# Performance work log

Measured on AMD Instinct MI355X. Metric: run time of the kernel, lower is better.

Reference implementation:

```python
import jax, jax.numpy as jnp
import numpy as np

# ---- Cl(3,0) algebra tables (basis: 1, e1, e2, e3, e12, e13, e23, e123) ----
def _build_algebra():
    dim = 8
    blades = sorted(range(dim), key=lambda b: (bin(b).count('1'), b))
    idx = {b: i for i, b in enumerate(blades)}
    C = np.zeros((dim, dim, dim), np.float32)
    for a in range(dim):
        for b in range(dim):
            s = 0; ash = a >> 1
            while ash:
                s += bin(ash & b).count('1'); ash >>= 1
            C[idx[a], idx[b], idx[a ^ b]] = -1.0 if (s & 1) else 1.0
    grades = np.array([bin(b).count('1') for b in blades])
    rev = np.array([(-1.0) ** (g * (g - 1) // 2) for g in grades], np.float32)
    gmask = np.zeros((4, dim), np.float32)
    gmask[grades, np.arange(dim)] = 1.0
    return C, rev, gmask, grades

_C_np, _REV_np, _GM_np, _GRADES = _build_algebra()
CAYLEY = jnp.asarray(_C_np)          # [8,8,8] sparse multiplication table
REV = jnp.asarray(_REV_np)           # reverse signs per blade
GMASK = jnp.asarray(_GM_np)          # [4,8] grade selector
BV_IDX = jnp.asarray(np.where(_GRADES == 2)[0])  # bivector slots [4,5,6]
G1_IDX = jnp.asarray(np.where(_GRADES == 1)[0])  # vector slots [1,2,3]

EPS = 1e-6
H_NUM, DEPTH, A_NUM, DISC, TEMP = 8, 3, 5, 0.99, 1.0

def gp(a, b):
    return jnp.einsum('...i,...j,ijk->...k', a, b, CAYLEY)

def reverse(x):
    return x * REV

def grade_energy(x):  # [...,8] -> [...,4] per-grade sum of squares
    return jnp.einsum('...d,gd->...g', x * x, GMASK)

def scatter_bv(c):  # [...,3] bivector coeffs -> full multivector [...,8]
    out = jnp.zeros(c.shape[:-1] + (8,), c.dtype)
    return out.at[..., BV_IDX].set(c)

def mv_exp_biv(b):  # exp of pure bivector in Cl(3,0): cos|B| + sinc|B| * B
    t = jnp.sqrt(jnp.sum(b * b, -1))
    small = t < 1e-6
    ts = jnp.where(small, 1.0, t)
    sinc = jnp.where(small, 1.0 - t * t / 6.0, jnp.sin(ts) / ts)
    return (sinc[..., None] * b).at[..., 0].add(jnp.cos(t))

def clayernorm(x, w):  # normalize by mean multivector norm across channels
    n = jnp.sqrt(jnp.sum(x * x, -1) + EPS)          # [...,C]
    denom = jnp.mean(n, -1, keepdims=True)[..., None] + EPS
    return x * w[:, None] / denom

def ggelu(x):  # gate multivector by GELU of its norm
    n = jnp.sqrt(jnp.sum(x * x, -1, keepdims=True) + EPS)
    return x * jax.nn.gelu(n) / (n + EPS)

def clinear(x, W, b):  # channel-mixing per blade: [O,C]x[...,C,8]
    return jnp.einsum('oc,...cd->...od', W, x) + b

def rotor_apply(x, bv):  # per-channel rotor sandwich, bv [C,3]
    R = mv_exp_biv(-0.5 * scatter_bv(bv))  # [C,8]
    return gp(gp(R, x), reverse(R))

def predict(x, nw, lw, lb, vw, vb, pw, pb):
    h = clayernorm(x, nw)
    h = clinear(h, lw, lb)
    h = ggelu(h)
    value = h[..., 0] @ vw + vb                      # grade-0 -> [N,1]
    g1 = h[..., G1_IDX].reshape(h.shape[0], -1)       # grade-1 flat
    policy = g1 @ pw + pb                             # [N,A]
    return policy, value

def dynamics(x, action, act_bv, nw, rbv, lw, lb, rw, rb):
    bv = act_bv[action]                               # [N,3]
    R = mv_exp_biv(-0.5 * scatter_bv(bv))[:, None, :]  # [N,1,8]
    ns = gp(gp(R, x), reverse(R))                     # rotor sandwich
    h = clayernorm(ns, nw)
    h = ggelu(h)
    h = rotor_apply(h, rbv)
    h = clinear(h, lw, lb)
    ns = ns + h                                       # residual GA block
    reward = ns[..., 0] @ rw + rb
    return reward, ns


def setup_inputs() -> dict:
    key = jax.random.key(0)
    ks = jax.random.split(key, 16)
    B, C, mid = 512, 256, 128
    f = jnp.float32
    return {
        'state': jax.random.normal(ks[0], (B, C, 8), f),
        'hyp_bv': jax.random.normal(ks[1], (H_NUM, 3), f) * 0.05,
        'sp_w1': jax.random.normal(ks[2], (4, 32), f) * 0.3,
        'sp_b1': jnp.zeros((32,), f),
        'sp_w2': jax.random.normal(ks[3], (32, 1), f) * 0.3,
        'sp_b2': jnp.zeros((1,), f),
        'p_norm_w': jnp.ones((C,), f),
        'p_lin_w': jax.random.normal(ks[4], (mid, C), f) / np.sqrt(C),
        'p_lin_b': jnp.zeros((mid, 8), f),
        'p_vw': jax.random.normal(ks[5], (mid, 1), f) * 0.1,
        'p_vb': jnp.zeros((1,), f),
        'p_pw': jax.random.normal(ks[6], (mid * 3, A_NUM), f) * 0.1,
        'p_pb': jnp.zeros((A_NUM,), f),
        'act_bv': jax.random.normal(ks[7], (A_NUM, 3), f) * 0.1,
        'd_norm_w': jnp.ones((C,), f),
        'd_rotor_bv': jax.random.normal(ks[8], (C, 3), f) * 0.05,
        'd_lin_w': jax.random.normal(ks[9], (C, C), f) / np.sqrt(C),
        'd_lin_b': jnp.zeros((C, 8), f),
        'd_rw': jax.random.normal(ks[10], (C, 1), f) * 0.1,
        'd_rb': jnp.zeros((1,), f),
    }


def reference(state, hyp_bv, sp_w1, sp_b1, sp_w2, sp_b2,
              p_norm_w, p_lin_w, p_lin_b, p_vw, p_vb, p_pw, p_pb,
              act_bv, d_norm_w, d_rotor_bv, d_lin_w, d_lin_b, d_rw, d_rb):
    B, C, D = state.shape
    H, A = H_NUM, A_NUM
    # hypothesis generation: H independent rotors applied to state
    R = mv_exp_biv(-0.5 * scatter_bv(hyp_bv))          # [H,8]
    hyp = gp(gp(R[None, :, None, :], state[:, None, :, :]),
             reverse(R)[None, :, None, :])             # [B,H,C,8]
    # exploration parameter from grade-norm features
    norms = jnp.sqrt(grade_energy(state) + 1e-12)       # [B,C,4]
    pooled = norms.mean(1)                              # [B,4]
    theta = jnp.maximum(pooled @ sp_w1 + sp_b1, 0.0) @ sp_w2 + sp_b2
    explore = jnp.abs(jnp.tanh(theta))                  # [B,1]
    N = B * H
    hf = hyp.reshape(N, C, D)
    exp_bh = jnp.broadcast_to(explore[:, None, :], (B, H, 1)).reshape(N, 1)
    noise = jax.random.normal(jax.random.key(42), (DEPTH, N, A), state.dtype) * 0.3
    hyp_values = jnp.zeros((B, H), state.dtype)
    first_actions = jnp.zeros((N,), jnp.int32)
    for d in range(DEPTH):  # fixed small depth loop; H vectorized
        policy, value = predict(hf, p_norm_w, p_lin_w, p_lin_b, p_vw, p_vb, p_pw, p_pb)
        bv_e = grade_energy(hf)[:, :, 2].mean(1, keepdims=True)  # bivector energy
        scores = policy + exp_bh * bv_e * noise[d]
        action = jnp.argmax(scores, -1)
        if d == 0:
            first_actions = action
        reward, hf = dynamics(hf, action, act_bv, d_norm_w, d_rotor_bv,
                              d_lin_w, d_lin_b, d_rw, d_rb)
        hyp_values = hyp_values + (DISC ** d) * reward.reshape(B, H)
    _, tv = predict(hf, p_norm_w, p_lin_w, p_lin_b, p_vw, p_vb, p_pw, p_pb)
    hyp_values = hyp_values + (DISC ** DEPTH) * tv.reshape(B, H)
    weights = jax.nn.softmax(hyp_values / TEMP, -1)     # [B,H]
    oh = jax.nn.one_hot(first_actions.reshape(B, H), A, dtype=state.dtype)
    ap = jnp.sum(weights[..., None] * oh, 1)            # [B,A]
    return ap / jnp.clip(jnp.sum(ap, -1, keepdims=True), 1e-8)
```

## Files before the change

### kernel.cpp

```cpp
#include <hip/hip_runtime.h>
#include <math.h>


#define NOISE_MODE 0
#define DEV static __device__ __forceinline__

constexpr int Bz = 512;
constexpr int Cz = 256;
constexpr int MIDz = 128;
constexpr int Hz = 8;
constexpr int Nz = 4096;
constexpr int Az = 5;
constexpr int NOISE_PER_D = Nz * Az;

constexpr size_t OFF_ROTH  = 0;
constexpr size_t OFF_ROTA  = OFF_ROTH + 64;
constexpr size_t OFF_ROTC  = OFF_ROTA + 40;
constexpr size_t OFF_EXPL  = OFF_ROTC + 2048;
constexpr size_t OFF_HV    = OFF_EXPL + 512;
constexpr size_t OFF_FIRST = OFF_HV + 4096;
constexpr size_t OFF_WTP   = OFF_FIRST + 4096;
constexpr size_t OFF_WTD   = OFF_WTP + (size_t)Cz * MIDz;
constexpr size_t OFF_A     = OFF_WTD + (size_t)Cz * Cz;

DEV void gp8(const float* a, const float* b, float* c) {
  c[0] = a[0]*b[0]+a[1]*b[1]+a[2]*b[2]+a[3]*b[3]-a[4]*b[4]-a[5]*b[5]-a[6]*b[6]-a[7]*b[7];
  c[1] = a[0]*b[1]+a[1]*b[0]-a[2]*b[4]-a[3]*b[5]+a[4]*b[2]+a[5]*b[3]-a[6]*b[7]-a[7]*b[6];
  c[2] = a[0]*b[2]+a[2]*b[0]+a[1]*b[4]-a[4]*b[1]-a[3]*b[6]+a[6]*b[3]+a[5]*b[7]+a[7]*b[5];
  c[3] = a[0]*b[3]+a[3]*b[0]+a[1]*b[5]-a[5]*b[1]+a[2]*b[6]-a[6]*b[2]-a[4]*b[7]-a[7]*b[4];
  c[4] = a[0]*b[4]+a[4]*b[0]+a[1]*b[2]-a[2]*b[1]-a[5]*b[6]+a[6]*b[5]+a[3]*b[7]+a[7]*b[3];
  c[5] = a[0]*b[5]+a[5]*b[0]+a[1]*b[3]-a[3]*b[1]+a[4]*b[6]-a[6]*b[4]-a[2]*b[7]-a[7]*b[2];
  c[6] = a[0]*b[6]+a[6]*b[0]+a[2]*b[3]-a[3]*b[2]-a[4]*b[5]+a[5]*b[4]+a[1]*b[7]+a[7]*b[1];
  c[7] = a[0]*b[7]+a[7]*b[0]+a[1]*b[6]+a[6]*b[1]+a[3]*b[4]+a[4]*b[3]-a[2]*b[5]-a[5]*b[2];
}

DEV void sandwich8(const float* R, const float* x, float* y) {
  float t[8];
  gp8(R, x, t);
  float Rr[8] = {R[0], R[1], R[2], R[3], -R[4], -R[5], -R[6], -R[7]};
  gp8(t, Rr, y);
}

DEV void rotor_from_bv(const float* bv, float* R) {
  float c4 = -0.5f * bv[0], c5 = -0.5f * bv[1], c6 = -0.5f * bv[2];
  float t = sqrtf(c4*c4 + c5*c5 + c6*c6);
  float sinc = (t < 1e-6f) ? (1.0f - t*t/6.0f) : (sinf(t)/t);
  R[0] = cosf(t); R[1] = 0.f; R[2] = 0.f; R[3] = 0.f;
  R[4] = sinc*c4; R[5] = sinc*c5; R[6] = sinc*c6; R[7] = 0.f;
}

DEV unsigned tf_rotl(unsigned v, int n) { return (v << n) | (v >> (32 - n)); }

DEV void threefry2x32(unsigned x0, unsigned x1, unsigned& o0, unsigned& o1) {
  const unsigned k0 = 0u, k1 = 42u;
  const unsigned k2 = k0 ^ k1 ^ 0x1BD11BDAu;
  x0 += k0; x1 += k1;
#define TF_R(r) { x0 += x1; x1 = tf_rotl(x1, r); x1 ^= x0; }
  TF_R(13) TF_R(15) TF_R(26) TF_R(6)
  x0 += k1; x1 += k2 + 1u;
  TF_R(17) TF_R(29) TF_R(16) TF_R(24)
  x0 += k2; x1 += k0 + 2u;
  TF_R(13) TF_R(15) TF_R(26) TF_R(6)
  x0 += k0; x1 += k1 + 3u;
  TF_R(17) TF_R(29) TF_R(16) TF_R(24)
  x0 += k1; x1 += k2 + 4u;
  TF_R(13) TF_R(15) TF_R(26) TF_R(6)
  x0 += k2; x1 += k0 + 5u;
#undef TF_R
  o0 = x0; o1 = x1;
}

DEV float erfinv32(float x) {
  float w = -log1pf(-x * x);
  float p;
  if (w < 5.0f) {
    w = w - 2.5f;
    p = 2.81022636e-08f;
    p = fmaf(p, w, 3.43273939e-07f);
    p = fmaf(p, w, -3.5233877e-06f);
    p = fmaf(p, w, -4.39150654e-06f);
    p = fmaf(p, w, 0.00021858087f);
    p = fmaf(p, w, -0.00125372503f);
    p = fmaf(p, w, -0.00417768164f);
    p = fmaf(p, w, 0.246640727f);
    p = fmaf(p, w, 1.50140941f);
  } else {
    w = sqrtf(w) - 3.0f;
    p = -0.000200214257f;
    p = fmaf(p, w, 0.000100950558f);
    p = fmaf(p, w, 0.00134934322f);
    p = fmaf(p, w, -0.00367342844f);
    p = fmaf(p, w, 0.00573950773f);
    p = fmaf(p, w, -0.0076224613f);
    p = fmaf(p, w, 0.00943887047f);
    p = fmaf(p, w, 1.00167406f);
    p = fmaf(p, w, 2.83297682f);
  }
  return p * x;
}

DEV float noise_val(int d, int r, int a) {
  unsigned idx = (unsigned)(d * NOISE_PER_D + r * Az + a);
  unsigned o0, o1, bits;
#if NOISE_MODE == 0
  threefry2x32(0u, idx, o0, o1);
  bits = o0 ^ o1;
#elif NOISE_MODE == 1
  const unsigned HALF = (unsigned)(3 * NOISE_PER_D) / 2u;
  unsigned j = (idx < HALF) ? idx : idx - HALF;
  threefry2x32(j, j + HALF, o0, o1);
  bits = (idx < HALF) ? o0 : o1;
#elif NOISE_MODE == 2
  threefry2x32(0u, idx, o0, o1);
  bits = o1;
#else
  threefry2x32(0u, idx, o0, o1);
  bits = o0;
#endif
  const float MINV = __uint_as_float(0xBF7FFFFFu);
  float f = __uint_as_float((bits >> 9) | 0x3F800000u) - 1.0f;
  float u = fmaxf(MINV, f * 2.0f + MINV);
  const float SQRT2 = __uint_as_float(0x3FB504F3u);
  return (SQRT2 * erfinv32(u)) * 0.3f;
}

DEV float gelu_tanh(float x) {
  float x3 = (x * x) * x;
  float t = tanhf(0.7978845608028654f * (x + 0.044715f * x3));
  return x * (0.5f * (1.0f + t));
}

DEV void pred_gemm(const float4* __restrict__ X, int l, float invd,
                   const float* __restrict__ WtP, const float* __restrict__ plb,
                   float hh[2][8]) {
  float pacc[2][8] = {{0,0,0,0,0,0,0,0},{0,0,0,0,0,0,0,0}};
  const float2* Wp2 = (const float2*)WtP;
#pragma unroll 4
  for (int c = 0; c < Cz; c++) {
    float4 xa = X[c], xb = X[Cz + c];
    float xv[8] = {xa.x, xa.y, xa.z, xa.w, xb.x, xb.y, xb.z, xb.w};
    float2 wv = Wp2[(size_t)c * 64 + l];
#pragma unroll
    for (int dd = 0; dd < 8; dd++) {
      pacc[0][dd] = fmaf(wv.x, xv[dd], pacc[0][dd]);
      pacc[1][dd] = fmaf(wv.y, xv[dd], pacc[1][dd]);
    }
  }
#pragma unroll
  for (int j = 0; j < 2; j++) {
    int o = 2 * l + j;
    float nsq = 0.f;
#pragma unroll
    for (int dd = 0; dd < 8; dd++) {
      hh[j][dd] = fmaf(pacc[j][dd], invd, plb[o * 8 + dd]);
      nsq += hh[j][dd] * hh[j][dd];
    }
    float nn = sqrtf(nsq + 1e-6f);
    float sc = gelu_tanh(nn) / (nn + 1e-6f);
#pragma unroll
    for (int dd = 0; dd < 8; dd++) hh[j][dd] *= sc;
  }
}


__global__ void k_prep(const float* __restrict__ hyp_bv, const float* __restrict__ act_bv,
                       const float* __restrict__ rot_bv, const float* __restrict__ plw,
                       const float* __restrict__ pnw, const float* __restrict__ dlw,
                       float* __restrict__ rotH, float* __restrict__ rotA,
                       float* __restrict__ rotC, float* __restrict__ hyp_val,
                       float* __restrict__ WtP, float* __restrict__ WtD) {
  int t = blockIdx.x * 256 + threadIdx.x;
  if (t < Cz * Cz)   { int c = t >> 8, o = t & 255; WtD[t] = dlw[o * Cz + c]; }
  if (t < Cz * MIDz) { int c = t >> 7, o = t & 127; WtP[t] = plw[o * Cz + c] * pnw[c]; }
  if (t < Nz) hyp_val[t] = 0.f;
  if (t < 8) rotor_from_bv(hyp_bv + t * 3, rotH + t * 8);
  else if (t < 13) rotor_from_bv(act_bv + (t - 8) * 3, rotA + (t - 8) * 8);
  else if (t >= 16 && t < 16 + Cz) rotor_from_bv(rot_bv + (t - 16) * 3, rotC + (t - 16) * 8);
}

__global__ void k_explore(const float* __restrict__ state, const float* __restrict__ w1,
                          const float* __restrict__ b1, const float* __restrict__ w2,
                          const float* __restrict__ b2, float* __restrict__ explore) {
  int b = blockIdx.x, c = threadIdx.x;
  const float4* xp = (const float4*)(state + ((size_t)b * Cz + c) * 8);
  float4 lo = xp[0], hi = xp[1];
  float g0 = lo.x * lo.x;
  float g1 = lo.y * lo.y + lo.z * lo.z + lo.w * lo.w;
  float g2 = hi.x * hi.x + hi.y * hi.y + hi.z * hi.z;
  float g3 = hi.w * hi.w;
  __shared__ float4 sm[256];
  sm[c] = make_float4(sqrtf(g0 + 1e-12f), sqrtf(g1 + 1e-12f),
                      sqrtf(g2 + 1e-12f), sqrtf(g3 + 1e-12f));
  __syncthreads();
  for (int s = 128; s > 0; s >>= 1) {
    if (c < s) {
      sm[c].x += sm[c + s].x; sm[c].y += sm[c + s].y;
      sm[c].z += sm[c + s].z; sm[c].w += sm[c + s].w;
    }
    __syncthreads();
  }
  if (c == 0) {
    float pooled[4] = {sm[0].x / 256.f, sm[0].y / 256.f, sm[0].z / 256.f, sm[0].w / 256.f};
    float theta = b2[0];
    for (int j = 0; j < 32; j++) {
      float hj = b1[j];
      for (int g = 0; g < 4; g++) hj = fmaf(pooled[g], w1[g * 32 + j], hj);
      hj = fmaxf(hj, 0.f);
      theta = fmaf(hj, w2[j], theta);
    }
    explore[b] = fabsf(tanhf(theta));
  }
}

__global__ __launch_bounds__(256, 4) void k_step(
    const float* __restrict__ src, float* __restrict__ dst, int apply_hyp,
    int dstep, int do_term,
    const float* __restrict__ rotH, const float* __restrict__ rotA,
    const float* __restrict__ rotC, const float* __restrict__ WtP,
    const float* __restrict__ plb, const float* __restrict__ pw,
    const float* __restrict__ pb, const float* __restrict__ vw,
    const float* __restrict__ vb, const float* __restrict__ dnw,
    const float* __restrict__ WtD, const float* __restrict__ dlb,
    const float* __restrict__ rw, const float* __restrict__ rb,
    const float* __restrict__ explore, float* __restrict__ hyp_val,
    int* __restrict__ first_act, float discf, float termdisc) {
  __shared__ float4 xs[4][2 * Cz];
  int w = threadIdx.x >> 6, l = threadIdx.x & 63;
  int r = blockIdx.x * 4 + w;
  int b = r >> 3, h = r & 7;
  float4* X = xs[w];
  const float* row = apply_hyp ? (src + (size_t)b * Cz * 8) : (src + (size_t)r * Cz * 8);
  float Rh[8];
  if (apply_hyp) {
#pragma unroll
    for (int i = 0; i < 8; i++) Rh[i] = rotH[h * 8 + i];
  }
  float nsum = 0.f, bsum = 0.f;
#pragma unroll
  for (int k = 0; k < 4; k++) {
    int c = 4 * l + k;
    const float4* xp = (const float4*)(row + (size_t)c * 8);
    float4 v0 = xp[0], v1 = xp[1];
    float x[8] = {v0.x, v0.y, v0.z, v0.w, v1.x, v1.y, v1.z, v1.w};
    if (apply_hyp) {
      float t[8];
      sandwich8(Rh, x, t);
#pragma unroll
      for (int i = 0; i < 8; i++) x[i] = t[i];
    }
    float ss = 0.f;
#pragma unroll
    for (int i = 0; i < 8; i++) ss += x[i] * x[i];
    nsum += sqrtf(ss + 1e-6f);
    bsum += x[4] * x[4] + x[5] * x[5] + x[6] * x[6];
    X[c]      = make_float4(x[0], x[1], x[2], x[3]);
    X[Cz + c] = make_float4(x[4], x[5], x[6], x[7]);
  }
#pragma unroll
  for (int m = 1; m < 64; m <<= 1) {
    nsum += __shfl_xor(nsum, m);
    bsum += __shfl_xor(bsum, m);
  }
  float invd = 1.0f / (nsum / 256.f + 1e-6f);
  float bv_e = bsum / 256.f;
  __syncthreads();

  float hh[2][8];
  pred_gemm(X, l, invd, WtP, plb, hh);
  float pol[Az] = {0, 0, 0, 0, 0};
#pragma unroll
  for (int j = 0; j < 2; j++) {
    int o = 2 * l + j;
#pragma unroll
    for (int k = 0; k < 3; k++) {
      float v = hh[j][1 + k];
      const float* pwj = pw + (size_t)(o * 3 + k) * Az;
#pragma unroll
      for (int a = 0; a < Az; a++) pol[a] = fmaf(v, pwj[a], pol[a]);
    }
  }
#pragma unroll
  for (int m = 1; m < 64; m <<= 1) {
#pragma unroll
    for (int a = 0; a < Az; a++) pol[a] += __shfl_xor(pol[a], m);
  }
  float coef = explore[b] * bv_e;
  float sa = -INFINITY;
  if (l < Az) sa = (pol[l] + pb[l]) + coef * noise_val(dstep, r, l);
  int best = 0;
  float bs = -INFINITY;
#pragma unroll
  for (int a = 0; a < Az; a++) {
    float s = __shfl(sa, a);
    if (s > bs) { bs = s; best = a; }
  }
  if (dstep == 0 && l == 0) first_act[r] = best;

  float Ra[8];
#pragma unroll
  for (int i = 0; i < 8; i++) Ra[i] = rotA[best * 8 + i];
  float y[4][8];
  float nsum2 = 0.f;
#pragma unroll
  for (int k = 0; k < 4; k++) {
    int c = 4 * l + k;
    float4 xa = X[c], xb = X[Cz + c];
    float x[8] = {xa.x, xa.y, xa.z, xa.w, xb.x, xb.y, xb.z, xb.w};
    sandwich8(Ra, x, y[k]);
    float ss = 0.f;
#pragma unroll
    for (int i = 0; i < 8; i++) ss += y[k][i] * y[k][i];
    nsum2 += sqrtf(ss + 1e-6f);
  }
#pragma unroll
  for (int m = 1; m < 64; m <<= 1) nsum2 += __shfl_xor(nsum2, m);
  float invd2 = 1.0f / (nsum2 / 256.f + 1e-6f);

#pragma unroll
  for (int k = 0; k < 4; k++) {
    int c = 4 * l + k;
    float sc = dnw[c] * invd2;
    float hch[8];
    float nsq = 0.f;
#pragma unroll
    for (int i = 0; i < 8; i++) { hch[i] = y[k][i] * sc; nsq += hch[i] * hch[i]; }
    float nn = sqrtf(nsq + 1e-6f);
    float ge = gelu_tanh(nn) / (nn + 1e-6f);
#pragma unroll
    for (int i = 0; i < 8; i++) hch[i] *= ge;
    float Rc[8];
    const float4* rp = (const float4*)(rotC + (size_t)c * 8);
    float4 r0 = rp[0], r1 = rp[1];
    Rc[0] = r0.x; Rc[1] = r0.y; Rc[2] = r0.z; Rc[3] = r0.w;
    Rc[4] = r1.x; Rc[5] = r1.y; Rc[6] = r1.z; Rc[7] = r1.w;
    float hp[8];
    sandwich8(Rc, hch, hp);
    X[c]      = make_float4(hp[0], hp[1], hp[2], hp[3]);
    X[Cz + c] = make_float4(hp[4], hp[5], hp[6], hp[7]);
  }
  __syncthreads();

  float acc[4][8];
#pragma unroll
  for (int g = 0; g < 4; g++) {
    int o = 4 * l + g;
#pragma unroll
    for (int dd = 0; dd < 8; dd++) acc[g][dd] = y[g][dd] + dlb[o * 8 + dd];
  }
  const float4* Wd4 = (const float4*)WtD;
#pragma unroll 4
  for (int c = 0; c < Cz; c++) {
    float4 xa = X[c], xb = X[Cz + c];
    float xv[8] = {xa.x, xa.y, xa.z, xa.w, xb.x, xb.y, xb.z, xb.w};
    float4 w4 = Wd4[(size_t)c * 64 + l];
#pragma unroll
    for (int dd = 0; dd < 8; dd++) {
      acc[0][dd] = fmaf(w4.x, xv[dd], acc[0][dd]);
      acc[1][dd] = fmaf(w4.y, xv[dd], acc[1][dd]);
      acc[2][dd] = fmaf(w4.z, xv[dd], acc[2][dd]);
      acc[3][dd] = fmaf(w4.w, xv[dd], acc[3][dd]);
    }
  }

  float rsum = 0.f;
  float hv_add;
  if (!do_term) {
    float* drow = dst + (size_t)r * Cz * 8;
#pragma unroll
    for (int g = 0; g < 4; g++) {
      int o = 4 * l + g;
      rsum = fmaf(acc[g][0], rw[o], rsum);
      float4* op = (float4*)(drow + (size_t)o * 8);
      op[0] = make_float4(acc[g][0], acc[g][1], acc[g][2], acc[g][3]);
      op[1] = make_float4(acc[g][4], acc[g][5], acc[g][6], acc[g][7]);
    }
#pragma unroll
    for (int m = 1; m < 64; m <<= 1) rsum += __shfl_xor(rsum, m);
    hv_add = discf * (rsum + rb[0]);
  } else {
    __syncthreads();
    float tsum = 0.f;
#pragma unroll
    for (int g = 0; g < 4; g++) {
      int o = 4 * l + g;
      rsum = fmaf(acc[g][0], rw[o], rsum);
      float ss = 0.f;
#pragma unroll
      for (int dd = 0; dd < 8; dd++) ss += acc[g][dd] * acc[g][dd];
      tsum += sqrtf(ss + 1e-6f);
      X[o]      = make_float4(acc[g][0], acc[g][1], acc[g][2], acc[g][3]);
      X[Cz + o] = make_float4(acc[g][4], acc[g][5], acc[g][6], acc[g][7]);
    }
#pragma unroll
    for (int m = 1; m < 64; m <<= 1) {
      rsum += __shfl_xor(rsum, m);
      tsum += __shfl_xor(tsum, m);
    }
    float invd3 = 1.0f / (tsum / 256.f + 1e-6f);
    __syncthreads();
    float th[2][8];
    pred_gemm(X, l, invd3, WtP, plb, th);
    float v = fmaf(th[0][0], vw[2 * l], th[1][0] * vw[2 * l + 1]);
#pragma unroll
    for (int m = 1; m < 64; m <<= 1) v += __shfl_xor(v, m);
    hv_add = discf * (rsum + rb[0]) + termdisc * (v + vb[0]);
  }
  if (l == 0) hyp_val[r] += hv_add;
}

__global__ void k_out(const float* __restrict__ hyp_val, const int* __restrict__ first_act,
                      float* __restrict__ out) {
  int b = blockIdx.x * blockDim.x + threadIdx.x;
  if (b >= Bz) return;
  float hv[Hz];
  float m = -INFINITY;
#pragma unroll
  for (int h = 0; h < Hz; h++) { hv[h] = hyp_val[b * Hz + h]; m = fmaxf(m, hv[h]); }
  float e[Hz];
  float se = 0.f;
#pragma unroll
  for (int h = 0; h < Hz; h++) { e[h] = expf(hv[h] - m); se += e[h]; }
  float ap[Az] = {0, 0, 0, 0, 0};
#pragma unroll
  for (int h = 0; h < Hz; h++) ap[first_act[b * Hz + h]] += e[h] / se;
  float tot = 0.f;
#pragma unroll
  for (int a = 0; a < Az; a++) tot += ap[a];
  float dn = fmaxf(tot, 1e-8f);
#pragma unroll
  for (int a = 0; a < Az; a++) out[b * Az + a] = ap[a] / dn;
}


extern "C" void kernel_launch(void* const* d_in, const int* in_sizes, int n_in,
                              void* d_out, int out_size, void* d_ws, size_t ws_size,
                              hipStream_t stream) {
  const float* state      = (const float*)d_in[0];
  const float* hyp_bv     = (const float*)d_in[1];
  const float* sp_w1      = (const float*)d_in[2];
  const float* sp_b1      = (const float*)d_in[3];
  const float* sp_w2      = (const float*)d_in[4];
  const float* sp_b2      = (const float*)d_in[5];
  const float* p_norm_w   = (const float*)d_in[6];
  const float* p_lin_w    = (const float*)d_in[7];
  const float* p_lin_b    = (const float*)d_in[8];
  const float* p_vw       = (const float*)d_in[9];
  const float* p_vb       = (const float*)d_in[10];
  const float* p_pw       = (const float*)d_in[11];
  const float* p_pb       = (const float*)d_in[12];
  const float* act_bv     = (const float*)d_in[13];
  const float* d_norm_w   = (const float*)d_in[14];
  const float* d_rotor_bv = (const float*)d_in[15];
  const float* d_lin_w    = (const float*)d_in[16];
  const float* d_lin_b    = (const float*)d_in[17];
  const float* d_rw       = (const float*)d_in[18];
  const float* d_rb       = (const float*)d_in[19];
  float* out = (float*)d_out;
  float* ws  = (float*)d_ws;

  float* rotH    = ws + OFF_ROTH;
  float* rotA    = ws + OFF_ROTA;
  float* rotC    = ws + OFF_ROTC;
  float* explore = ws + OFF_EXPL;
  float* hyp_val = ws + OFF_HV;
  int*   first   = (int*)(ws + OFF_FIRST);
  float* WtP     = ws + OFF_WTP;
  float* WtD     = ws + OFF_WTD;
  float* bufA    = ws + OFF_A;

  k_prep<<<256, 256, 0, stream>>>(hyp_bv, act_bv, d_rotor_bv, p_lin_w, p_norm_w,
                                  d_lin_w, rotH, rotA, rotC, hyp_val, WtP, WtD);
  k_explore<<<Bz, 256, 0, stream>>>(state, sp_w1, sp_b1, sp_w2, sp_b2, explore);

  const float d1 = 0.99f, d2 = 0.99f * 0.99f, d3 = 0.99f * 0.99f * 0.99f;
  k_step<<<Nz / 4, 256, 0, stream>>>(state, bufA, 1, 0, 0, rotH, rotA, rotC, WtP,
                                     p_lin_b, p_pw, p_pb, p_vw, p_vb, d_norm_w, WtD,
                                     d_lin_b, d_rw, d_rb, explore, hyp_val, first,
                                     1.0f, 0.f);
  k_step<<<Nz / 4, 256, 0, stream>>>(bufA, bufA, 0, 1, 0, rotH, rotA, rotC, WtP,
                                     p_lin_b, p_pw, p_pb, p_vw, p_vb, d_norm_w, WtD,
                                     d_lin_b, d_rw, d_rb, explore, hyp_val, first,
                                     d1, 0.f);
  k_step<<<Nz / 4, 256, 0, stream>>>(bufA, bufA, 0, 2, 1, rotH, rotA, rotC, WtP,
                                     p_lin_b, p_pw, p_pb, p_vw, p_vb, d_norm_w, WtD,
                                     d_lin_b, d_rw, d_rb, explore, hyp_val, first,
                                     d2, d3);
  k_out<<<2, 256, 0, stream>>>(hyp_val, first, out);
}
```

Before: 379.1 us.

## Fuse three depth-step kernels into one persistent search kernel with strided LDS layout

Merges the three per-depth k_step launches into a single k_search kernel. Each wavefront now keeps its hypothesis state in LDS across all depth steps, so the global round trip of the intermediate state buffer and the hyp_val zero-init are gone, along with two launches. It also changes the LDS channel layout to a strided (k*64+l) index so per-lane writes and GEMM reads touch different banks. The GEMM loops are restructured to match the new layout. The cost is a longer-running kernel whose register pressure may change.

```diff
diff --git a/kernel.cpp b/kernel.cpp
--- a/kernel.cpp
+++ b/kernel.cpp
@@ -21,7 +21,6 @@
 constexpr size_t OFF_FIRST = OFF_HV + 4096;
 constexpr size_t OFF_WTP   = OFF_FIRST + 4096;
 constexpr size_t OFF_WTD   = OFF_WTP + (size_t)Cz * MIDz;
-constexpr size_t OFF_A     = OFF_WTD + (size_t)Cz * Cz;
 
 DEV void gp8(const float* a, const float* b, float* c) {
   c[0] = a[0]*b[0]+a[1]*b[1]+a[2]*b[2]+a[3]*b[3]-a[4]*b[4]-a[5]*b[5]-a[6]*b[6]-a[7]*b[7];
@@ -133,26 +132,42 @@
 DEV void pred_gemm(const float4* __restrict__ X, int l, float invd,
                    const float* __restrict__ WtP, const float* __restrict__ plb,
                    float hh[2][8]) {
-  float pacc[2][8] = {{0,0,0,0,0,0,0,0},{0,0,0,0,0,0,0,0}};
+  float a0[8] = {0, 0, 0, 0, 0, 0, 0, 0};
+  float a1[8] = {0, 0, 0, 0, 0, 0, 0, 0};
   const float2* Wp2 = (const float2*)WtP;
-#pragma unroll 4
-  for (int c = 0; c < Cz; c++) {
-    float4 xa = X[c], xb = X[Cz + c];
-    float xv[8] = {xa.x, xa.y, xa.z, xa.w, xb.x, xb.y, xb.z, xb.w};
-    float2 wv = Wp2[(size_t)c * 64 + l];
-#pragma unroll
-    for (int dd = 0; dd < 8; dd++) {
-      pacc[0][dd] = fmaf(wv.x, xv[dd], pacc[0][dd]);
-      pacc[1][dd] = fmaf(wv.y, xv[dd], pacc[1][dd]);
+#pragma unroll 2
+  for (int c4 = 0; c4 < 64; c4++) {
+#pragma unroll
+    for (int k = 0; k < 4; k++) {
+      float4 xa = X[(k << 6) + c4];
+      float4 xb = X[Cz + (k << 6) + c4];
+      float2 wv = Wp2[(size_t)(4 * c4 + k) * 64 + l];
+      a0[0] = fmaf(wv.x, xa.x, a0[0]);
+      a0[1] = fmaf(wv.x, xa.y, a0[1]);
+      a0[2] = fmaf(wv.x, xa.z, a0[2]);
+      a0[3] = fmaf(wv.x, xa.w, a0[3]);
+      a0[4] = fmaf(wv.x, xb.x, a0[4]);
+      a0[5] = fmaf(wv.x, xb.y, a0[5]);
+      a0[6] = fmaf(wv.x, xb.z, a0[6]);
+      a0[7] = fmaf(wv.x, xb.w, a0[7]);
+      a1[0] = fmaf(wv.y, xa.x, a1[0]);
+      a1[1] = fmaf(wv.y, xa.y, a1[1]);
+      a1[2] = fmaf(wv.y, xa.z, a1[2]);
+      a1[3] = fmaf(wv.y, xa.w, a1[3]);
+      a1[4] = fmaf(wv.y, xb.x, a1[4]);
+      a1[5] = fmaf(wv.y, xb.y, a1[5]);
+      a1[6] = fmaf(wv.y, xb.z, a1[6]);
+      a1[7] = fmaf(wv.y, xb.w, a1[7]);
     }
   }
 #pragma unroll
   for (int j = 0; j < 2; j++) {
     int o = 2 * l + j;
+    const float* aj = (j == 0) ? a0 : a1;
     float nsq = 0.f;
 #pragma unroll
     for (int dd = 0; dd < 8; dd++) {
-      hh[j][dd] = fmaf(pacc[j][dd], invd, plb[o * 8 + dd]);
+      hh[j][dd] = fmaf(aj[dd], invd, plb[o * 8 + dd]);
       nsq += hh[j][dd] * hh[j][dd];
     }
     float nn = sqrtf(nsq + 1e-6f);
@@ -167,12 +182,11 @@
                        const float* __restrict__ rot_bv, const float* __restrict__ plw,
                        const float* __restrict__ pnw, const float* __restrict__ dlw,
                        float* __restrict__ rotH, float* __restrict__ rotA,
-                       float* __restrict__ rotC, float* __restrict__ hyp_val,
-                       float* __restrict__ WtP, float* __restrict__ WtD) {
+                       float* __restrict__ rotC, float* __restrict__ WtP,
+                       float* __restrict__ WtD) {
   int t = blockIdx.x * 256 + threadIdx.x;
   if (t < Cz * Cz)   { int c = t >> 8, o = t & 255; WtD[t] = dlw[o * Cz + c]; }
   if (t < Cz * MIDz) { int c = t >> 7, o = t & 127; WtP[t] = plw[o * Cz + c] * pnw[c]; }
-  if (t < Nz) hyp_val[t] = 0.f;
   if (t < 8) rotor_from_bv(hyp_bv + t * 3, rotH + t * 8);
   else if (t < 13) rotor_from_bv(act_bv + (t - 8) * 3, rotA + (t - 8) * 8);
   else if (t >= 16 && t < 16 + Cz) rotor_from_bv(rot_bv + (t - 16) * 3, rotC + (t - 16) * 8);
@@ -212,9 +226,8 @@
   }
 }
 
-__global__ __launch_bounds__(256, 4) void k_step(
-    const float* __restrict__ src, float* __restrict__ dst, int apply_hyp,
-    int dstep, int do_term,
+__global__ __launch_bounds__(256, 4) void k_search(
+    const float* __restrict__ state,
     const float* __restrict__ rotH, const float* __restrict__ rotA,
     const float* __restrict__ rotC, const float* __restrict__ WtP,
     const float* __restrict__ plb, const float* __restrict__ pw,
@@ -223,163 +236,155 @@
     const float* __restrict__ WtD, const float* __restrict__ dlb,
     const float* __restrict__ rw, const float* __restrict__ rb,
     const float* __restrict__ explore, float* __restrict__ hyp_val,
-    int* __restrict__ first_act, float discf, float termdisc) {
+    int* __restrict__ first_act) {
   __shared__ float4 xs[4][2 * Cz];
   int w = threadIdx.x >> 6, l = threadIdx.x & 63;
   int r = blockIdx.x * 4 + w;
   int b = r >> 3, h = r & 7;
   float4* X = xs[w];
-  const float* row = apply_hyp ? (src + (size_t)b * Cz * 8) : (src + (size_t)r * Cz * 8);
+  const float* row = state + (size_t)b * Cz * 8;
   float Rh[8];
-  if (apply_hyp) {
-#pragma unroll
-    for (int i = 0; i < 8; i++) Rh[i] = rotH[h * 8 + i];
-  }
+#pragma unroll
+  for (int i = 0; i < 8; i++) Rh[i] = rotH[h * 8 + i];
+
   float nsum = 0.f, bsum = 0.f;
 #pragma unroll
   for (int k = 0; k < 4; k++) {
     int c = 4 * l + k;
     const float4* xp = (const float4*)(row + (size_t)c * 8);
     float4 v0 = xp[0], v1 = xp[1];
-    float x[8] = {v0.x, v0.y, v0.z, v0.w, v1.x, v1.y, v1.z, v1.w};
-    if (apply_hyp) {
-      float t[8];
-      sandwich8(Rh, x, t);
-#pragma unroll
-      for (int i = 0; i < 8; i++) x[i] = t[i];
-    }
+    float xin[8] = {v0.x, v0.y, v0.z, v0.w, v1.x, v1.y, v1.z, v1.w};
+    float x[8];
+    sandwich8(Rh, xin, x);
     float ss = 0.f;
 #pragma unroll
     for (int i = 0; i < 8; i++) ss += x[i] * x[i];
     nsum += sqrtf(ss + 1e-6f);
     bsum += x[4] * x[4] + x[5] * x[5] + x[6] * x[6];
-    X[c]      = make_float4(x[0], x[1], x[2], x[3]);
-    X[Cz + c] = make_float4(x[4], x[5], x[6], x[7]);
+    int sl = (k << 6) + l;
+    X[sl]      = make_float4(x[0], x[1], x[2], x[3]);
+    X[Cz + sl] = make_float4(x[4], x[5], x[6], x[7]);
   }
 #pragma unroll
   for (int m = 1; m < 64; m <<= 1) {
     nsum += __shfl_xor(nsum, m);
     bsum += __shfl_xor(bsum, m);
   }
-  float invd = 1.0f / (nsum / 256.f + 1e-6f);
-  float bv_e = bsum / 256.f;
-  __syncthreads();
-
-  float hh[2][8];
-  pred_gemm(X, l, invd, WtP, plb, hh);
-  float pol[Az] = {0, 0, 0, 0, 0};
-#pragma unroll
-  for (int j = 0; j < 2; j++) {
-    int o = 2 * l + j;
-#pragma unroll
-    for (int k = 0; k < 3; k++) {
-      float v = hh[j][1 + k];
-      const float* pwj = pw + (size_t)(o * 3 + k) * Az;
-#pragma unroll
-      for (int a = 0; a < Az; a++) pol[a] = fmaf(v, pwj[a], pol[a]);
-    }
-  }
-#pragma unroll
-  for (int m = 1; m < 64; m <<= 1) {
-#pragma unroll
-    for (int a = 0; a < Az; a++) pol[a] += __shfl_xor(pol[a], m);
-  }
-  float coef = explore[b] * bv_e;
-  float sa = -INFINITY;
-  if (l < Az) sa = (pol[l] + pb[l]) + coef * noise_val(dstep, r, l);
-  int best = 0;
-  float bs = -INFINITY;
-#pragma unroll
-  for (int a = 0; a < Az; a++) {
-    float s = __shfl(sa, a);
-    if (s > bs) { bs = s; best = a; }
-  }
-  if (dstep == 0 && l == 0) first_act[r] = best;
-
-  float Ra[8];
-#pragma unroll
-  for (int i = 0; i < 8; i++) Ra[i] = rotA[best * 8 + i];
-  float y[4][8];
-  float nsum2 = 0.f;
-#pragma unroll
-  for (int k = 0; k < 4; k++) {
-    int c = 4 * l + k;
-    float4 xa = X[c], xb = X[Cz + c];
-    float x[8] = {xa.x, xa.y, xa.z, xa.w, xb.x, xb.y, xb.z, xb.w};
-    sandwich8(Ra, x, y[k]);
-    float ss = 0.f;
-#pragma unroll
-    for (int i = 0; i < 8; i++) ss += y[k][i] * y[k][i];
-    nsum2 += sqrtf(ss + 1e-6f);
-  }
-#pragma unroll
-  for (int m = 1; m < 64; m <<= 1) nsum2 += __shfl_xor(nsum2, m);
-  float invd2 = 1.0f / (nsum2 / 256.f + 1e-6f);
-
-#pragma unroll
-  for (int k = 0; k < 4; k++) {
-    int c = 4 * l + k;
-    float sc = dnw[c] * invd2;
-    float hch[8];
-    float nsq = 0.f;
-#pragma unroll
-    for (int i = 0; i < 8; i++) { hch[i] = y[k][i] * sc; nsq += hch[i] * hch[i]; }
-    float nn = sqrtf(nsq + 1e-6f);
-    float ge = gelu_tanh(nn) / (nn + 1e-6f);
-#pragma unroll
-    for (int i = 0; i < 8; i++) hch[i] *= ge;
-    float Rc[8];
-    const float4* rp = (const float4*)(rotC + (size_t)c * 8);
-    float4 r0 = rp[0], r1 = rp[1];
-    Rc[0] = r0.x; Rc[1] = r0.y; Rc[2] = r0.z; Rc[3] = r0.w;
-    Rc[4] = r1.x; Rc[5] = r1.y; Rc[6] = r1.z; Rc[7] = r1.w;
-    float hp[8];
-    sandwich8(Rc, hch, hp);
-    X[c]      = make_float4(hp[0], hp[1], hp[2], hp[3]);
-    X[Cz + c] = make_float4(hp[4], hp[5], hp[6], hp[7]);
-  }
-  __syncthreads();
-
-  float acc[4][8];
-#pragma unroll
-  for (int g = 0; g < 4; g++) {
-    int o = 4 * l + g;
-#pragma unroll
-    for (int dd = 0; dd < 8; dd++) acc[g][dd] = y[g][dd] + dlb[o * 8 + dd];
-  }
-  const float4* Wd4 = (const float4*)WtD;
-#pragma unroll 4
-  for (int c = 0; c < Cz; c++) {
-    float4 xa = X[c], xb = X[Cz + c];
-    float xv[8] = {xa.x, xa.y, xa.z, xa.w, xb.x, xb.y, xb.z, xb.w};
-    float4 w4 = Wd4[(size_t)c * 64 + l];
-#pragma unroll
-    for (int dd = 0; dd < 8; dd++) {
-      acc[0][dd] = fmaf(w4.x, xv[dd], acc[0][dd]);
-      acc[1][dd] = fmaf(w4.y, xv[dd], acc[1][dd]);
-      acc[2][dd] = fmaf(w4.z, xv[dd], acc[2][dd]);
-      acc[3][dd] = fmaf(w4.w, xv[dd], acc[3][dd]);
-    }
-  }
-
-  float rsum = 0.f;
-  float hv_add;
-  if (!do_term) {
-    float* drow = dst + (size_t)r * Cz * 8;
+
+  float coefE = explore[b];
+  float hv = 0.f, disc = 1.0f;
+  int firstb = 0;
+
+#pragma unroll 1
+  for (int d = 0; d < 3; d++) {
+    float invd = 1.0f / (nsum / 256.f + 1e-6f);
+    float bv_e = bsum / 256.f;
+    __syncthreads();
+
+    float hh[2][8];
+    pred_gemm(X, l, invd, WtP, plb, hh);
+    float pol[Az] = {0, 0, 0, 0, 0};
+#pragma unroll
+    for (int j = 0; j < 2; j++) {
+      int o = 2 * l + j;
+#pragma unroll
+      for (int k = 0; k < 3; k++) {
+        float v = hh[j][1 + k];
+        const float* pwj = pw + (size_t)(o * 3 + k) * Az;
+#pragma unroll
+        for (int a = 0; a < Az; a++) pol[a] = fmaf(v, pwj[a], pol[a]);
+      }
+    }
+#pragma unroll
+    for (int m = 1; m < 64; m <<= 1) {
+#pragma unroll
+      for (int a = 0; a < Az; a++) pol[a] += __shfl_xor(pol[a], m);
+    }
+    float sa = -INFINITY;
+    if (l < Az) sa = (pol[l] + pb[l]) + coefE * bv_e * noise_val(d, r, l);
+    int best = 0;
+    float bs = -INFINITY;
+#pragma unroll
+    for (int a = 0; a < Az; a++) {
+      float s = __shfl(sa, a);
+      if (s > bs) { bs = s; best = a; }
+    }
+    if (d == 0) firstb = best;
+
+    float Ra[8];
+#pragma unroll
+    for (int i = 0; i < 8; i++) Ra[i] = rotA[best * 8 + i];
+    float y[4][8];
+    float nsum2 = 0.f;
+#pragma unroll
+    for (int k = 0; k < 4; k++) {
+      int sl = (k << 6) + l;
+      float4 xa = X[sl], xb = X[Cz + sl];
+      float x[8] = {xa.x, xa.y, xa.z, xa.w, xb.x, xb.y, xb.z, xb.w};
+      sandwich8(Ra, x, y[k]);
+      float ss = 0.f;
+#pragma unroll
+      for (int i = 0; i < 8; i++) ss += y[k][i] * y[k][i];
+      nsum2 += sqrtf(ss + 1e-6f);
+    }
+#pragma unroll
+    for (int m = 1; m < 64; m <<= 1) nsum2 += __shfl_xor(nsum2, m);
+    float invd2 = 1.0f / (nsum2 / 256.f + 1e-6f);
+
+#pragma unroll
+    for (int k = 0; k < 4; k++) {
+      int c = 4 * l + k;
+      float sc = dnw[c] * invd2;
+      float hch[8];
+      float nsq = 0.f;
+#pragma unroll
+      for (int i = 0; i < 8; i++) { hch[i] = y[k][i] * sc; nsq += hch[i] * hch[i]; }
+      float nn = sqrtf(nsq + 1e-6f);
+      float ge = gelu_tanh(nn) / (nn + 1e-6f);
+#pragma unroll
+      for (int i = 0; i < 8; i++) hch[i] *= ge;
+      float Rc[8];
+      const float4* rp = (const float4*)(rotC + (size_t)c * 8);
+      float4 r0 = rp[0], r1 = rp[1];
+      Rc[0] = r0.x; Rc[1] = r0.y; Rc[2] = r0.z; Rc[3] = r0.w;
+      Rc[4] = r1.x; Rc[5] = r1.y; Rc[6] = r1.z; Rc[7] = r1.w;
+      float hp[8];
+      sandwich8(Rc, hch, hp);
+      int sl = (k << 6) + l;
+      X[sl]      = make_float4(hp[0], hp[1], hp[2], hp[3]);
+      X[Cz + sl] = make_float4(hp[4], hp[5], hp[6], hp[7]);
+    }
+    __syncthreads();
+
+    float acc[4][8];
 #pragma unroll
     for (int g = 0; g < 4; g++) {
       int o = 4 * l + g;
-      rsum = fmaf(acc[g][0], rw[o], rsum);
-      float4* op = (float4*)(drow + (size_t)o * 8);
-      op[0] = make_float4(acc[g][0], acc[g][1], acc[g][2], acc[g][3]);
-      op[1] = make_float4(acc[g][4], acc[g][5], acc[g][6], acc[g][7]);
-    }
-#pragma unroll
-    for (int m = 1; m < 64; m <<= 1) rsum += __shfl_xor(rsum, m);
-    hv_add = discf * (rsum + rb[0]);
-  } else {
-    __syncthreads();
-    float tsum = 0.f;
+#pragma unroll
+      for (int dd = 0; dd < 8; dd++) acc[g][dd] = y[g][dd] + dlb[o * 8 + dd];
+    }
+    const float4* Wd4 = (const float4*)WtD;
+#pragma unroll 2
+    for (int c4 = 0; c4 < 64; c4++) {
+#pragma unroll
+      for (int k = 0; k < 4; k++) {
+        float4 xa = X[(k << 6) + c4];
+        float4 xb = X[Cz + (k << 6) + c4];
+        float xv[8] = {xa.x, xa.y, xa.z, xa.w, xb.x, xb.y, xb.z, xb.w};
+        float4 w4 = Wd4[(size_t)(4 * c4 + k) * 64 + l];
+#pragma unroll
+        for (int dd = 0; dd < 8; dd++) {
+          acc[0][dd] = fmaf(w4.x, xv[dd], acc[0][dd]);
+          acc[1][dd] = fmaf(w4.y, xv[dd], acc[1][dd]);
+          acc[2][dd] = fmaf(w4.z, xv[dd], acc[2][dd]);
+          acc[3][dd] = fmaf(w4.w, xv[dd], acc[3][dd]);
+        }
+      }
+    }
+
+    float rsum = 0.f;
+    nsum = 0.f;
+    bsum = 0.f;
 #pragma unroll
     for (int g = 0; g < 4; g++) {
       int o = 4 * l + g;
@@ -387,25 +392,35 @@
       float ss = 0.f;
 #pragma unroll
       for (int dd = 0; dd < 8; dd++) ss += acc[g][dd] * acc[g][dd];
-      tsum += sqrtf(ss + 1e-6f);
-      X[o]      = make_float4(acc[g][0], acc[g][1], acc[g][2], acc[g][3]);
-      X[Cz + o] = make_float4(acc[g][4], acc[g][5], acc[g][6], acc[g][7]);
+      nsum += sqrtf(ss + 1e-6f);
+      bsum += acc[g][4] * acc[g][4] + acc[g][5] * acc[g][5] + acc[g][6] * acc[g][6];
+      int sl = (g << 6) + l;
+      X[sl]      = make_float4(acc[g][0], acc[g][1], acc[g][2], acc[g][3]);
+      X[Cz + sl] = make_float4(acc[g][4], acc[g][5], acc[g][6], acc[g][7]);
     }
 #pragma unroll
     for (int m = 1; m < 64; m <<= 1) {
       rsum += __shfl_xor(rsum, m);
-      tsum += __shfl_xor(tsum, m);
-    }
-    float invd3 = 1.0f / (tsum / 256.f + 1e-6f);
-    __syncthreads();
-    float th[2][8];
-    pred_gemm(X, l, invd3, WtP, plb, th);
-    float v = fmaf(th[0][0], vw[2 * l], th[1][0] * vw[2 * l + 1]);
-#pragma unroll
-    for (int m = 1; m < 64; m <<= 1) v += __shfl_xor(v, m);
-    hv_add = discf * (rsum + rb[0]) + termdisc * (v + vb[0]);
-  }
-  if (l == 0) hyp_val[r] += hv_add;
+      nsum += __shfl_xor(nsum, m);
+      bsum += __shfl_xor(bsum, m);
+    }
+    hv += disc * (rsum + rb[0]);
+    disc *= 0.99f;
+  }
+
+  float invd3 = 1.0f / (nsum / 256.f + 1e-6f);
+  __syncthreads();
+  float th[2][8];
+  pred_gemm(X, l, invd3, WtP, plb, th);
+  float v = fmaf(th[0][0], vw[2 * l], th[1][0] * vw[2 * l + 1]);
+#pragma unroll
+  for (int m = 1; m < 64; m <<= 1) v += __shfl_xor(v, m);
+  hv += disc * (v + vb[0]);
+
+  if (l == 0) {
+    hyp_val[r] = hv;
+    first_act[r] = firstb;
+  }
 }
 
 __global__ void k_out(const float* __restrict__ hyp_val, const int* __restrict__ first_act,
@@ -466,24 +481,12 @@
   int*   first   = (int*)(ws + OFF_FIRST);
   float* WtP     = ws + OFF_WTP;
   float* WtD     = ws + OFF_WTD;
-  float* bufA    = ws + OFF_A;
 
   k_prep<<<256, 256, 0, stream>>>(hyp_bv, act_bv, d_rotor_bv, p_lin_w, p_norm_w,
-                                  d_lin_w, rotH, rotA, rotC, hyp_val, WtP, WtD);
+                                  d_lin_w, rotH, rotA, rotC, WtP, WtD);
   k_explore<<<Bz, 256, 0, stream>>>(state, sp_w1, sp_b1, sp_w2, sp_b2, explore);
-
-  const float d1 = 0.99f, d2 = 0.99f * 0.99f, d3 = 0.99f * 0.99f * 0.99f;
-  k_step<<<Nz / 4, 256, 0, stream>>>(state, bufA, 1, 0, 0, rotH, rotA, rotC, WtP,
-                                     p_lin_b, p_pw, p_pb, p_vw, p_vb, d_norm_w, WtD,
-                                     d_lin_b, d_rw, d_rb, explore, hyp_val, first,
-                                     1.0f, 0.f);
-  k_step<<<Nz / 4, 256, 0, stream>>>(bufA, bufA, 0, 1, 0, rotH, rotA, rotC, WtP,
-                                     p_lin_b, p_pw, p_pb, p_vw, p_vb, d_norm_w, WtD,
-                                     d_lin_b, d_rw, d_rb, explore, hyp_val, first,
-                                     d1, 0.f);
-  k_step<<<Nz / 4, 256, 0, stream>>>(bufA, bufA, 0, 2, 1, rotH, rotA, rotC, WtP,
-                                     p_lin_b, p_pw, p_pb, p_vw, p_vb, d_norm_w, WtD,
-                                     d_lin_b, d_rw, d_rb, explore, hyp_val, first,
-                                     d2, d3);
+  k_search<<<Nz / 4, 256, 0, stream>>>(state, rotH, rotA, rotC, WtP, p_lin_b,
+                                       p_pw, p_pb, p_vw, p_vb, d_norm_w, WtD,
+                                       d_lin_b, d_rw, d_rb, explore, hyp_val, first);
   k_out<<<2, 256, 0, stream>>>(hyp_val, first, out);
 }
```

New measurement: 572.7 us. +51.1%, slower.
